# Optimization experiments

Hardware: AMD Instinct MI355X
Metric: run time of the kernel (lower is better)

## Reference

```python
import jax, jax.numpy as jnp
import numpy as np

B, S, M, KD, VD, QD, H, NQ = 256, 200, 32, 128, 256, 128, 64, 10000
TA, TB, TC = 0.075, 0.088, 1.0  # triangular membership params a, b, c


def setup_inputs() -> dict:
    key = jax.random.key(0)
    ks = jax.random.split(key, 12)
    q_data = jax.random.randint(ks[0], (B, S), 0, NQ + 1)
    # kaiming-normal-ish embedding table; padding_idx=0 row zeroed
    q_embed_weight = jax.random.normal(ks[1], (NQ + 1, QD)) * np.sqrt(2.0 / QD)
    q_embed_weight = q_embed_weight.at[0].set(0.0)
    key_mem = jax.random.normal(ks[2], (M, KD)) * np.sqrt(2.0 / KD)
    value_mem = jax.random.normal(ks[3], (M, VD)) * np.sqrt(2.0 / VD)
    in_dim = VD + QD
    s = 1.0 / np.sqrt(H)
    W_ih = jax.random.uniform(ks[4], (4 * H, in_dim), minval=-s, maxval=s)
    W_hh = jax.random.uniform(ks[5], (4 * H, H), minval=-s, maxval=s)
    b_ih = jax.random.uniform(ks[6], (4 * H,), minval=-s, maxval=s)
    b_hh = jax.random.uniform(ks[7], (4 * H,), minval=-s, maxval=s)
    W_pred = jax.random.normal(ks[8], (1, H)) * np.sqrt(2.0 / H)
    b_pred = jnp.zeros((1,))
    init_h = jax.random.normal(ks[9], (B, H))
    init_c = jax.random.normal(ks[10], (B, H))
    return dict(q_data=q_data, q_embed_weight=q_embed_weight, key_mem=key_mem,
                value_mem=value_mem, W_ih=W_ih, W_hh=W_hh, b_ih=b_ih, b_hh=b_hh,
                W_pred=W_pred, b_pred=b_pred, init_h=init_h, init_c=init_c)


def triangular_layer(cw):
    """cw: [N, M] correlation weights -> [N] unique-row indices.
    Faithful to torch: trit-quantize each weight {0,1,2}, then map each row to its
    index in the (lexicographically sorted) unique-row table, which is exactly what
    the pairwise squared-distance matmul + (dist==0).nonzero() trick computes."""
    w = jnp.minimum((cw - TA) / (TB - TA), (TC - cw) / (TC - TB))
    w = jnp.maximum(w, 0.0)
    iv = jnp.where(w >= 0.6, 2, jnp.where(w >= 0.1, 1, 0)).astype(jnp.int32)  # [N, M]
    # pack 32 trits into two int32 keys (3^16 < 2^31)
    p = jnp.power(3, jnp.arange(16, dtype=jnp.int32))  # [16]
    kh = (iv[:, :16] * p).sum(1)
    kl = (iv[:, 16:] * p).sum(1)
    order = jnp.lexsort((kl, kh))  # primary key kh
    kh_s, kl_s = kh[order], kl[order]
    change = jnp.concatenate([jnp.zeros((1,), jnp.int32),
                              ((kh_s[1:] != kh_s[:-1]) | (kl_s[1:] != kl_s[:-1])).astype(jnp.int32)])
    rank_sorted = jnp.cumsum(change)
    inv = jnp.zeros(cw.shape[0], jnp.int32).at[order].set(rank_sorted)
    return inv


def reference(q_data, q_embed_weight, key_mem, value_mem, W_ih, W_hh, b_ih, b_hh,
              W_pred, b_pred, init_h, init_c):
    q_emb = q_embed_weight[q_data]                                  # [B,S,QD]
    cw = jax.nn.softmax(jnp.einsum('bsd,md->bsm', q_emb, key_mem))  # DKVMN attention
    read = jnp.einsum('bsm,mv->bsv', cw, value_mem)                 # [B,S,VD]
    ids = triangular_layer(cw.reshape(B * S, M))                    # [B*S]
    x = jnp.concatenate([read, q_emb], axis=-1)                     # [B,S,VD+QD]

    def step(carry, xt):
        h, c = carry
        g = xt @ W_ih.T + h @ W_hh.T + b_ih + b_hh
        i, f, gg, o = jnp.split(g, 4, axis=-1)
        c = jax.nn.sigmoid(f) * c + jax.nn.sigmoid(i) * jnp.tanh(gg)
        h = jax.nn.sigmoid(o) * jnp.tanh(c)
        return (h, c), h

    _, hs = jax.lax.scan(step, (init_h, init_c), jnp.swapaxes(x, 0, 1))
    hs = jnp.swapaxes(hs, 0, 1)                                     # [B,S,H]
    pred = jax.nn.sigmoid(hs @ W_pred.T + b_pred)[..., 0]           # [B,S]
    return pred, ids
```

## Files before the change

kernel.cpp:

```cpp
#include <hip/hip_runtime.h>

#define BB 256
#define SS 200
#define MM 32
#define KDIM 128
#define VDIM 256
#define QDIM 128
#define HH 64
#define NROWS 10001
#define NSAMP (BB*SS)
#define INDIM (VDIM+QDIM)
#define DHS 8192
#define DHMASK (DHS-1)
#define XR 16
#define CH 50
#define NB_ATTN 2501

typedef unsigned long long u64;
typedef unsigned int u32;

__device__ __forceinline__ float fexp(float x){ return __builtin_amdgcn_exp2f(x * 1.44269504f); }
__device__ __forceinline__ float fsigm(float x){ return __builtin_amdgcn_rcpf(1.f + fexp(-x)); }
__device__ __forceinline__ float ftanh(float x){ return 1.f - 2.f*__builtin_amdgcn_rcpf(1.f + fexp(2.f*x)); }
__device__ __forceinline__ int clampq(int q){ return q < 0 ? 0 : (q > NROWS-1 ? NROWS-1 : q); }

__device__ __forceinline__ u32 hash64(u64 x){
  x ^= x >> 33; x *= 0xff51afd7ed558ccdULL;
  x ^= x >> 33; x *= 0xc4ceb9fe1a85ec53ULL;
  x ^= x >> 33;
  return (u32)x;
}

__device__ __forceinline__ u64 shflx64(u64 v, int m){
  int lo = __shfl_xor((int)(u32)v, m, 64);
  int hi = __shfl_xor((int)(u32)(v >> 32), m, 64);
  return ((u64)(u32)hi << 32) | (u32)lo;
}

__global__ void k_tr(const float* __restrict__ W_ih, const float* __restrict__ key_mem,
                     float* __restrict__ WQT4, float* __restrict__ KT,
                     float* __restrict__ WVT, u32* __restrict__ present){
  int idx = blockIdx.x*256 + threadIdx.x;
  if (idx < 131072) {
    int dd = idx & 3, j = (idx >> 2) & 255, d4 = idx >> 10;
    WQT4[idx] = W_ih[j*INDIM + VDIM + 4*d4 + dd];
  } else if (idx < 135168) {
    int t = idx - 131072;
    int m = t & 31, d = t >> 5; KT[t] = key_mem[m*KDIM + d];
  } else if (idx < 200704) {
    int t = idx - 135168;
    int j = t & 255, v = t >> 8; WVT[v*256 + j] = W_ih[j*INDIM + v];
  } else {
    int t = idx - 200704;
    if (t < NROWS) present[t] = 0u;
  }
}

__global__ __launch_bounds__(256) void k_front(
    const float* __restrict__ emb, const float* __restrict__ KT,
    const float* __restrict__ val, const float* __restrict__ WVT,
    const int* __restrict__ q_data,
    float* __restrict__ CW, u64* __restrict__ KEYT,
    float* __restrict__ VW, u32* __restrict__ present){
  int bid = blockIdx.x;
  if (bid < NB_ATTN) {
    int w = threadIdx.x >> 6, l = threadIdx.x & 63;
    int n = bid*4 + w;
    __shared__ float se[4][QDIM];
    bool valid = (n < NROWS);
    if (valid) {
      se[w][l]      = emb[n*QDIM + l];
      se[w][l + 64] = emb[n*QDIM + l + 64];
    }
    __syncthreads();
    int m = l & 31;
    float logit = 0.f;
    if (valid && l < 32)
      for (int d = 0; d < KDIM; ++d) logit += se[w][d] * KT[d*32 + m];
    float mx = logit;
    #pragma unroll
    for (int msk = 16; msk >= 1; msk >>= 1) mx = fmaxf(mx, __shfl_xor(mx, msk, 64));
    float e = (l < 32) ? expf(logit - mx) : 0.f;
    float sum = e;
    #pragma unroll
    for (int msk = 16; msk >= 1; msk >>= 1) sum += __shfl_xor(sum, msk, 64);
    float cw = e / sum;
    float wv = fminf((cw - 0.075f)/0.013f, (1.0f - cw)/0.912f);
    wv = fmaxf(wv, 0.f);
    int iv = (wv >= 0.6f) ? 2 : ((wv >= 0.1f) ? 1 : 0);
    int ee = (m < 16) ? m + 16 : m - 16;
    u64 p3 = 1;
    for (int i = 0; i < 31; ++i) if (i < ee) p3 *= 3ULL;
    u64 term = (valid && l < 32) ? (u64)iv * p3 : 0ULL;
    #pragma unroll
    for (int msk = 16; msk >= 1; msk >>= 1) term += shflx64(term, msk);
    if (valid && l < 32) CW[n*256 + m] = cw;
    if (valid && l == 0) KEYT[n] = term;
  } else if (bid < NB_ATTN + MM) {
    int m = bid - NB_ATTN, j = threadIdx.x;
    __shared__ float sval[VDIM];
    sval[j] = val[m*VDIM + j];
    __syncthreads();
    float a0=0.f, a1=0.f, a2=0.f, a3=0.f;
    for (int v = 0; v < VDIM; v += 4) {
      a0 += sval[v+0]*WVT[(v+0)*256 + j];
      a1 += sval[v+1]*WVT[(v+1)*256 + j];
      a2 += sval[v+2]*WVT[(v+2)*256 + j];
      a3 += sval[v+3]*WVT[(v+3)*256 + j];
    }
    VW[m*256 + j] = (a0+a1)+(a2+a3);
  } else {
    int i = (bid - NB_ATTN - MM)*256 + threadIdx.x;
    if (i < NSAMP) present[clampq(q_data[i])] = 1u;
  }
}

__global__ __launch_bounds__(256) void k_xw(
    const float* __restrict__ CW, const float* __restrict__ emb,
    const float* __restrict__ VW, const float* __restrict__ WQT4,
    const float* __restrict__ b_ih, const float* __restrict__ b_hh,
    float* __restrict__ XW4){
  int base = blockIdx.x * XR;
  int j = threadIdx.x;
  __shared__ float scw[XR][32];
  __shared__ __align__(16) float ses[XR][QDIM];
  for (int idx = j; idx < XR*32; idx += 256) {
    int r = idx >> 5, m = idx & 31, n = base + r;
    scw[r][m] = (n < NROWS) ? CW[n*256 + m] : 0.f;
  }
  for (int idx = j; idx < XR*QDIM; idx += 256) {
    int r = idx >> 7, d = idx & 127, n = base + r;
    ses[r][d] = (n < NROWS) ? emb[n*QDIM + d] : 0.f;
  }
  __syncthreads();
  float bias = b_ih[j] + b_hh[j];
  float acc[XR];
  #pragma unroll
  for (int r = 0; r < XR; ++r) acc[r] = bias;
  for (int m = 0; m < MM; ++m) {
    float wv = VW[m*256 + j];
    #pragma unroll
    for (int r = 0; r < XR; ++r) acc[r] += scw[r][m] * wv;
  }
  for (int d4 = 0; d4 < QDIM/4; ++d4) {
    float4 wq = *(const float4*)(WQT4 + d4*1024 + j*4);
    #pragma unroll
    for (int r = 0; r < XR; ++r) {
      float4 ev = *(const float4*)(&ses[r][4*d4]);
      acc[r] += ev.x*wq.x + ev.y*wq.y + ev.z*wq.z + ev.w*wq.w;
    }
  }
  int gate = j >> 6, unit = j & 63;
  #pragma unroll
  for (int r = 0; r < XR; ++r)
    if (base + r < NROWS) XW4[(size_t)(base + r)*256 + 4*unit + gate] = acc[r];
}

__global__ __launch_bounds__(1024) void k_dedup(
    const u32* __restrict__ present, const u64* __restrict__ KEYT,
    u32* __restrict__ g_htab, u32* __restrict__ g_pay,
    u32* __restrict__ counter, u64* __restrict__ uniq){
  __shared__ u32 sh_tab[DHS];
  __shared__ u32 sh_pay[DHS];
  __shared__ u32 sh_cnt;
  int tid = threadIdx.x;
  for (int i = tid; i < DHS; i += 1024) sh_tab[i] = 0u;
  if (tid == 0) sh_cnt = 0u;
  __syncthreads();
  for (int n = tid; n < NROWS; n += 1024) {
    if (present[n] != 1u) continue;
    u64 key = KEYT[n];
    u32 h = hash64(key) & DHMASK;
    while (true) {
      u32 cur = sh_tab[h];
      if (cur != 0u) {
        if (KEYT[cur-1u] == key) break;
        h = (h + 1) & DHMASK; continue;
      }
      u32 prev = atomicCAS(&sh_tab[h], 0u, (u32)(n + 1));
      if (prev == 0u) {
        u32 idx = atomicAdd(&sh_cnt, 1u);
        uniq[idx] = key;
        sh_pay[h] = idx;
        break;
      }
      if (KEYT[prev-1u] == key) break;
      h = (h + 1) & DHMASK;
    }
  }
  __syncthreads();
  for (int i = tid; i < DHS; i += 1024) {
    u32 v = sh_tab[i];
    g_htab[i] = v;
    g_pay[i]  = v ? sh_pay[i] : 0u;
  }
  if (tid == 0) *counter = sh_cnt;
}

__global__ __launch_bounds__(256) void k_rank(const u64* __restrict__ uniq,
                                              const u32* __restrict__ counter,
                                              u32* __restrict__ RANK){
  __shared__ u64 chunk[2048];
  u32 U = *counter;
  int u = blockIdx.x*256 + threadIdx.x;
  u64 mykey = (u < (int)U) ? uniq[u] : 0;
  u32 cnt = 0;
  for (u32 base = 0; base < U; base += 2048) {
    u32 n = (U - base < 2048u) ? (U - base) : 2048u;
    __syncthreads();
    for (u32 t = threadIdx.x; t < n; t += 256) chunk[t] = uniq[base + t];
    __syncthreads();
    if (u < (int)U)
      for (u32 j = 0; j < n; ++j) cnt += (chunk[j] < mykey) ? 1u : 0u;
  }
  if (u < (int)U) RANK[u] = cnt;
}

__global__ void k_qrank(const u32* __restrict__ present, const u64* __restrict__ KEYT,
                        const u32* __restrict__ g_htab, const u32* __restrict__ g_pay,
                        const u32* __restrict__ RANK, u32* __restrict__ RANKQ){
  int n = blockIdx.x*blockDim.x + threadIdx.x;
  if (n >= NROWS || present[n] != 1u) return;
  u64 key = KEYT[n];
  u32 h = hash64(key) & DHMASK;
  while (true) {
    u32 cur = g_htab[h];
    if (cur != 0u && KEYT[cur-1u] == key) { RANKQ[n] = RANK[g_pay[h]]; return; }
    h = (h + 1) & DHMASK;
  }
}

__global__ void k_ids(const int* __restrict__ q_data, const u32* __restrict__ RANKQ,
                      float* __restrict__ out_ids){
  int i = blockIdx.x*blockDim.x + threadIdx.x;
  if (i >= NSAMP) return;
  out_ids[i] = (float)RANKQ[clampq(q_data[i])];
}

__global__ __launch_bounds__(256, 1) void k_lstm(
    const int* __restrict__ q_data, const float* __restrict__ XW4,
    const float* __restrict__ W_hh,
    const float* __restrict__ W_pred, const float* __restrict__ b_pred,
    const float* __restrict__ init_h, const float* __restrict__ init_c,
    float* __restrict__ out_pred){
  const int b = blockIdx.x, t = threadIdx.x;
  const int w = t >> 6, l = t & 63;
  const int g = l >> 4, u = l & 15;
  const int unit = w*16 + u;
  __shared__ float XWc[CH][256];
  __shared__ __align__(16) float Hbuf[SS][68];
  __shared__ float swp[HH];
  __shared__ int   sq[SS];
  for (int s = t; s < SS; s += 256) sq[s] = clampq(q_data[b*SS + s]);
  if (t < HH) swp[t] = W_pred[t];

  float wgt[HH];
  {
    const float4* wr = (const float4*)(W_hh + (size_t)(g*HH + unit)*HH);
    #pragma unroll
    for (int j4 = 0; j4 < HH/4; ++j4) {
      float4 v = wr[j4];
      wgt[4*j4+0]=v.x; wgt[4*j4+1]=v.y; wgt[4*j4+2]=v.z; wgt[4*j4+3]=v.w;
    }
  }
  float hfull[HH];
  {
    const float4* ih = (const float4*)(init_h + b*HH);
    #pragma unroll
    for (int j4 = 0; j4 < HH/4; ++j4) {
      float4 v = ih[j4];
      hfull[4*j4+0]=v.x; hfull[4*j4+1]=v.y; hfull[4*j4+2]=v.z; hfull[4*j4+3]=v.w;
    }
  }
  float c  = init_c[b*HH + unit];
  float bp = b_pred[0];
  __syncthreads();

  for (int cs = 0; cs < SS; cs += CH) {
    for (int rr = w; rr < CH; rr += 4) {
      float4 xv = *(const float4*)(XW4 + (size_t)sq[cs + rr]*256 + 4*l);
      int wp = l >> 4, up = l & 15;
      XWc[rr][wp*64 +  0 + up] = xv.x;
      XWc[rr][wp*64 + 16 + up] = xv.y;
      XWc[rr][wp*64 + 32 + up] = xv.z;
      XWc[rr][wp*64 + 48 + up] = xv.w;
    }
    __syncthreads();
    for (int sl = 0; sl < CH; ++sl) {
      const int s = cs + sl;
      float a0=0.f, a1=0.f, a2=0.f, a3=0.f;
      #pragma unroll
      for (int j = 0; j < 16; ++j) {
        a0 += wgt[j   ]*hfull[j   ];
        a1 += wgt[j+16]*hfull[j+16];
        a2 += wgt[j+32]*hfull[j+32];
        a3 += wgt[j+48]*hfull[j+48];
      }
      float a = XWc[sl][w*64 + l] + ((a0+a1)+(a2+a3));
      float v0 = a;
      float v1 = __shfl_xor(a, 16, 64);
      float v2 = __shfl_xor(a, 32, 64);
      float v3 = __shfl_xor(v1, 32, 64);
      float vv[4] = {v0, v1, v2, v3};
      float ii = vv[g], ff = vv[g^1], gg = vv[g^2], oo = vv[g^3];
      c = fsigm(ff)*c + fsigm(ii)*ftanh(gg);
      float hh = fsigm(oo)*ftanh(c);
      if (g == 0) Hbuf[s][unit] = hh;
      __syncthreads();
      const float4* hb = (const float4*)(&Hbuf[s][0]);
      #pragma unroll
      for (int j4 = 0; j4 < HH/4; ++j4) {
        float4 v = hb[j4];
        hfull[4*j4+0]=v.x; hfull[4*j4+1]=v.y; hfull[4*j4+2]=v.z; hfull[4*j4+3]=v.w;
      }
    }
  }
  __syncthreads();
  if (t < SS) {
    float acc = 0.f;
    #pragma unroll 16
    for (int kk = 0; kk < HH; ++kk) {
      int k2 = (kk + t) & 63;
      acc += Hbuf[t][k2] * swp[k2];
    }
    out_pred[b*SS + t] = fsigm(acc + bp);
  }
}

extern "C" void kernel_launch(void* const* d_in, const int* in_sizes, int n_in,
                              void* d_out, int out_size, void* d_ws, size_t ws_size,
                              hipStream_t stream) {
  const int*   q_data  = (const int*)d_in[0];
  const float* emb     = (const float*)d_in[1];
  const float* keym    = (const float*)d_in[2];
  const float* val     = (const float*)d_in[3];
  const float* W_ih    = (const float*)d_in[4];
  const float* W_hh    = (const float*)d_in[5];
  const float* b_ih    = (const float*)d_in[6];
  const float* b_hh    = (const float*)d_in[7];
  const float* W_pred  = (const float*)d_in[8];
  const float* b_pred  = (const float*)d_in[9];
  const float* init_h  = (const float*)d_in[10];
  const float* init_c  = (const float*)d_in[11];

  char* ws = (char*)d_ws;
  float* XW4     = (float*)(ws + 0);
  float* VW      = (float*)(ws + 10241024);
  u64*  KEYT     = (u64*) (ws + 10273792);
  u64*  uniq     = (u64*) (ws + 10353920);
  u32*  RANK     = (u32*) (ws + 10434048);
  u32*  g_htab   = (u32*) (ws + 10474240);
  u32*  g_pay    = (u32*) (ws + 10507008);
  u32*  counter  = (u32*) (ws + 10539776);
  u32*  present  = (u32*) (ws + 10539840);
  u32*  RANKQ    = (u32*) (ws + 10579904);
  float* WQT4    = (float*)(ws + 10619968);
  float* KT      = (float*)(ws + 11144256);
  float* WVT     = (float*)(ws + 11160640);
  float* CW      = XW4;

  float* out_pred = (float*)d_out;
  float* out_ids  = out_pred + NSAMP;

  hipLaunchKernelGGL(k_tr,    dim3(824), dim3(256), 0, stream,
                     W_ih, keym, WQT4, KT, WVT, present);
  hipLaunchKernelGGL(k_front, dim3(NB_ATTN + MM + 200), dim3(256), 0, stream,
                     emb, KT, val, WVT, q_data, CW, KEYT, VW, present);
  hipLaunchKernelGGL(k_dedup, dim3(1), dim3(1024), 0, stream,
                     present, KEYT, g_htab, g_pay, counter, uniq);
  hipLaunchKernelGGL(k_rank,  dim3((NROWS+255)/256), dim3(256), 0, stream, uniq, counter, RANK);
  hipLaunchKernelGGL(k_qrank, dim3((NROWS+255)/256), dim3(256), 0, stream,
                     present, KEYT, g_htab, g_pay, RANK, RANKQ);
  hipLaunchKernelGGL(k_xw,    dim3((NROWS+XR-1)/XR), dim3(256), 0, stream,
                     CW, emb, VW, WQT4, b_ih, b_hh, XW4);
  hipLaunchKernelGGL(k_ids,   dim3((NSAMP+255)/256), dim3(256), 0, stream, q_data, RANKQ, out_ids);
  hipLaunchKernelGGL(k_lstm,  dim3(BB), dim3(256), 0, stream,
                     q_data, XW4, W_hh, W_pred, b_pred, init_h, init_c, out_pred);
}
```

Baseline: 275.3 us.

## Run LSTM recurrence with one wave per batch computing all four gates

Rewrites the LSTM kernel to use a single 64-thread wave per batch row, where each thread holds all four gate weight rows and computes i,f,g,o for its hidden unit. This removes the cross-lane shuffles and makes the per-step block barrier a single-wave sync. The LDS chunk staging of input projections is replaced with a two-step-ahead register prefetch. The cost is four times more FMAs per thread per step and about 320 live weight/state registers, with a risk of spills or a longer dependent chain per step.

```diff
diff --git a/kernel.cpp b/kernel.cpp
--- a/kernel.cpp
+++ b/kernel.cpp
@@ -13,7 +13,6 @@
 #define DHS 8192
 #define DHMASK (DHS-1)
 #define XR 16
-#define CH 50
 #define NB_ATTN 2501
 
 typedef unsigned long long u64;
@@ -237,30 +236,33 @@
   out_ids[i] = (float)RANKQ[clampq(q_data[i])];
 }
 
-__global__ __launch_bounds__(256, 1) void k_lstm(
+__global__ __launch_bounds__(64, 1) void k_lstm(
     const int* __restrict__ q_data, const float* __restrict__ XW4,
     const float* __restrict__ W_hh,
     const float* __restrict__ W_pred, const float* __restrict__ b_pred,
     const float* __restrict__ init_h, const float* __restrict__ init_c,
     float* __restrict__ out_pred){
-  const int b = blockIdx.x, t = threadIdx.x;
-  const int w = t >> 6, l = t & 63;
-  const int g = l >> 4, u = l & 15;
-  const int unit = w*16 + u;
-  __shared__ float XWc[CH][256];
+  const int b = blockIdx.x;
+  const int u = threadIdx.x;
   __shared__ __align__(16) float Hbuf[SS][68];
+  __shared__ int   sq[SS];
   __shared__ float swp[HH];
-  __shared__ int   sq[SS];
-  for (int s = t; s < SS; s += 256) sq[s] = clampq(q_data[b*SS + s]);
-  if (t < HH) swp[t] = W_pred[t];
-
-  float wgt[HH];
+
+  for (int s = u; s < SS; s += 64) sq[s] = clampq(q_data[b*SS + s]);
+  swp[u] = W_pred[u];
+
+  float wi[HH], wf[HH], wg[HH], wo[HH];
   {
-    const float4* wr = (const float4*)(W_hh + (size_t)(g*HH + unit)*HH);
+    const float4* r0 = (const float4*)(W_hh + (size_t)(0*HH + u)*HH);
+    const float4* r1 = (const float4*)(W_hh + (size_t)(1*HH + u)*HH);
+    const float4* r2 = (const float4*)(W_hh + (size_t)(2*HH + u)*HH);
+    const float4* r3 = (const float4*)(W_hh + (size_t)(3*HH + u)*HH);
     #pragma unroll
     for (int j4 = 0; j4 < HH/4; ++j4) {
-      float4 v = wr[j4];
-      wgt[4*j4+0]=v.x; wgt[4*j4+1]=v.y; wgt[4*j4+2]=v.z; wgt[4*j4+3]=v.w;
+      float4 a = r0[j4]; wi[4*j4]=a.x; wi[4*j4+1]=a.y; wi[4*j4+2]=a.z; wi[4*j4+3]=a.w;
+      float4 e = r1[j4]; wf[4*j4]=e.x; wf[4*j4+1]=e.y; wf[4*j4+2]=e.z; wf[4*j4+3]=e.w;
+      float4 f = r2[j4]; wg[4*j4]=f.x; wg[4*j4+1]=f.y; wg[4*j4+2]=f.z; wg[4*j4+3]=f.w;
+      float4 g = r3[j4]; wo[4*j4]=g.x; wo[4*j4+1]=g.y; wo[4*j4+2]=g.z; wo[4*j4+3]=g.w;
     }
   }
   float hfull[HH];
@@ -272,58 +274,46 @@
       hfull[4*j4+0]=v.x; hfull[4*j4+1]=v.y; hfull[4*j4+2]=v.z; hfull[4*j4+3]=v.w;
     }
   }
-  float c  = init_c[b*HH + unit];
+  float c  = init_c[b*HH + u];
   float bp = b_pred[0];
   __syncthreads();
 
-  for (int cs = 0; cs < SS; cs += CH) {
-    for (int rr = w; rr < CH; rr += 4) {
-      float4 xv = *(const float4*)(XW4 + (size_t)sq[cs + rr]*256 + 4*l);
-      int wp = l >> 4, up = l & 15;
-      XWc[rr][wp*64 +  0 + up] = xv.x;
-      XWc[rr][wp*64 + 16 + up] = xv.y;
-      XWc[rr][wp*64 + 32 + up] = xv.z;
-      XWc[rr][wp*64 + 48 + up] = xv.w;
-    }
-    __syncthreads();
-    for (int sl = 0; sl < CH; ++sl) {
-      const int s = cs + sl;
-      float a0=0.f, a1=0.f, a2=0.f, a3=0.f;
-      #pragma unroll
-      for (int j = 0; j < 16; ++j) {
-        a0 += wgt[j   ]*hfull[j   ];
-        a1 += wgt[j+16]*hfull[j+16];
-        a2 += wgt[j+32]*hfull[j+32];
-        a3 += wgt[j+48]*hfull[j+48];
-      }
-      float a = XWc[sl][w*64 + l] + ((a0+a1)+(a2+a3));
-      float v0 = a;
-      float v1 = __shfl_xor(a, 16, 64);
-      float v2 = __shfl_xor(a, 32, 64);
-      float v3 = __shfl_xor(v1, 32, 64);
-      float vv[4] = {v0, v1, v2, v3};
-      float ii = vv[g], ff = vv[g^1], gg = vv[g^2], oo = vv[g^3];
-      c = fsigm(ff)*c + fsigm(ii)*ftanh(gg);
-      float hh = fsigm(oo)*ftanh(c);
-      if (g == 0) Hbuf[s][unit] = hh;
-      __syncthreads();
-      const float4* hb = (const float4*)(&Hbuf[s][0]);
-      #pragma unroll
-      for (int j4 = 0; j4 < HH/4; ++j4) {
-        float4 v = hb[j4];
-        hfull[4*j4+0]=v.x; hfull[4*j4+1]=v.y; hfull[4*j4+2]=v.z; hfull[4*j4+3]=v.w;
-      }
-    }
-  }
-  __syncthreads();
-  if (t < SS) {
+  float4 xwA = *(const float4*)(XW4 + (size_t)sq[0]*256 + 4*u);
+  float4 xwB = *(const float4*)(XW4 + (size_t)sq[1]*256 + 4*u);
+
+  for (int s = 0; s < SS; ++s) {
+    int sp = (s + 2 < SS) ? s + 2 : SS - 1;
+    float4 xwC = *(const float4*)(XW4 + (size_t)sq[sp]*256 + 4*u);
+    float ai = 0.f, af = 0.f, ag = 0.f, ao = 0.f;
+    #pragma unroll
+    for (int j = 0; j < HH; ++j) {
+      ai += wi[j]*hfull[j];
+      af += wf[j]*hfull[j];
+      ag += wg[j]*hfull[j];
+      ao += wo[j]*hfull[j];
+    }
+    ai += xwA.x; af += xwA.y; ag += xwA.z; ao += xwA.w;
+    c = fsigm(af)*c + fsigm(ai)*ftanh(ag);
+    float hh = fsigm(ao)*ftanh(c);
+    Hbuf[s][u] = hh;
+    __syncthreads();
+    const float4* hb = (const float4*)(&Hbuf[s][0]);
+    #pragma unroll
+    for (int j4 = 0; j4 < HH/4; ++j4) {
+      float4 v = hb[j4];
+      hfull[4*j4+0]=v.x; hfull[4*j4+1]=v.y; hfull[4*j4+2]=v.z; hfull[4*j4+3]=v.w;
+    }
+    xwA = xwB; xwB = xwC;
+  }
+
+  for (int s = u; s < SS; s += 64) {
     float acc = 0.f;
     #pragma unroll 16
     for (int kk = 0; kk < HH; ++kk) {
-      int k2 = (kk + t) & 63;
-      acc += Hbuf[t][k2] * swp[k2];
-    }
-    out_pred[b*SS + t] = fsigm(acc + bp);
+      int k2 = (kk + u) & 63;
+      acc += Hbuf[s][k2] * swp[k2];
+    }
+    out_pred[b*SS + s] = fsigm(acc + bp);
   }
 }
 
@@ -374,6 +364,6 @@
   hipLaunchKernelGGL(k_xw,    dim3((NROWS+XR-1)/XR), dim3(256), 0, stream,
                      CW, emb, VW, WQT4, b_ih, b_hh, XW4);
   hipLaunchKernelGGL(k_ids,   dim3((NSAMP+255)/256), dim3(256), 0, stream, q_data, RANKQ, out_ids);
-  hipLaunchKernelGGL(k_lstm,  dim3(BB), dim3(256), 0, stream,
+  hipLaunchKernelGGL(k_lstm,  dim3(BB), dim3(64), 0, stream,
                      q_data, XW4, W_hh, W_pred, b_pred, init_h, init_c, out_pred);
 }
```

Result: slower. 363.4 us (+32.0%).
